# Optimization experiments

Hardware: AMD Instinct MI355X
Metric: run time of the kernel (lower is better)

The kernel has to match this reference:

```python
import jax, jax.numpy as jnp
import numpy as np

CUTOFF = 5.0
CUTOFF_ANGLE = 3.5
N = 25000
E = 800000
EA = 300000
T = 1600000
NBASIS = 8          # default radial basis size (bessel)
NBASIS_ANG = 8
DIM = 256
DIM_SRC = 64
DIM_DST = 32
DIM_ANGLE = 8
NMAX_ANGLE = 4
SPECIES_DIM = 16
NSPEC = 50


def bessel_basis(r, rc, n):
    # sin(k*pi*r/rc)/r Bessel-type radial basis, k=1..n  -> [E, n]
    x = r[:, None]
    k = jnp.arange(1, n + 1, dtype=r.dtype)[None, :] * (np.pi / rc)
    return jnp.sqrt(2.0 / rc) * jnp.sin(k * x) / x


def tssr2(x):
    # two-sided smooth square-root activation (identity inside |x|<=1)
    ax = jnp.abs(x)
    return jnp.where(ax <= 1.0, x, jnp.sign(x) * (2.0 * jnp.sqrt(jnp.maximum(ax, 1.0)) - 1.0))


def setup_inputs() -> dict:
    key = jax.random.key(0)
    ks = jax.random.split(key, 24)
    species = jax.random.randint(ks[0], (N,), 1, 17)
    edge_src = jax.random.randint(ks[1], (E,), 0, N)
    edge_dst = jax.random.randint(ks[2], (E,), 0, N)
    distances = 0.5 + jax.random.uniform(ks[3], (E,)) * (CUTOFF - 0.5)
    switch = 0.5 + 0.5 * jnp.cos(np.pi * distances / CUTOFF)
    angles = jax.random.uniform(ks[4], (T,)) * np.pi
    angle_src = jax.random.randint(ks[5], (T,), 0, EA)
    angle_dst = jax.random.randint(ks[6], (T,), 0, EA)
    central_atom = jax.random.randint(ks[7], (T,), 0, N)
    distances_angle = 0.5 + jax.random.uniform(ks[8], (EA,)) * (CUTOFF_ANGLE - 0.5)
    switch_angle = 0.5 + 0.5 * jnp.cos(np.pi * distances_angle / CUTOFF_ANGLE)
    s = lambda k, sh, scale: jax.random.normal(k, sh, jnp.float32) * scale
    din0 = SPECIES_DIM + DIM_SRC + NBASIS * DIM_DST + (NMAX_ANGLE + 1) * DIM_ANGLE  # 376
    din1 = DIM + DIM_SRC + NBASIS * DIM_DST + (NMAX_ANGLE + 1) * DIM_ANGLE          # 616
    return {
        'species': species, 'edge_src': edge_src, 'edge_dst': edge_dst,
        'distances': distances, 'switch': switch,
        'angles': angles, 'angle_src': angle_src, 'angle_dst': angle_dst,
        'central_atom': central_atom, 'distances_angle': distances_angle,
        'switch_angle': switch_angle,
        'species_table': s(ks[9], (NSPEC, SPECIES_DIM), 1.0),
        'W_si0': s(ks[10], (SPECIES_DIM, DIM_SRC + DIM_DST), SPECIES_DIM ** -0.5),
        'W_si1': s(ks[11], (DIM, DIM_SRC + DIM_DST), DIM ** -0.5),
        'W_da0': s(ks[12], (NBASIS_ANG, DIM_ANGLE), NBASIS_ANG ** -0.5),
        'W_da1': s(ks[13], (NBASIS_ANG, DIM_ANGLE), NBASIS_ANG ** -0.5),
        'W_mix0': s(ks[14], (din0, DIM), din0 ** -0.5),
        'b_mix0': jnp.zeros((DIM,), jnp.float32),
        'W_mix1': s(ks[15], (din1, DIM), din1 ** -0.5),
        'b_mix1': jnp.zeros((DIM,), jnp.float32),
    }


def reference(species, edge_src, edge_dst, distances, switch, angles, angle_src,
              angle_dst, central_atom, distances_angle, switch_angle,
              species_table, W_si0, W_si1, W_da0, W_da1,
              W_mix0, b_mix0, W_mix1, b_mix1):
    n_atoms = species.shape[0]
    # species encoding (learned/random table lookup)
    xi = species_table[species]                                   # [N, 16]
    # radial embeddings, smoothly switched at cutoff
    rb = bessel_basis(distances, CUTOFF, NBASIS) * switch[:, None]            # [E, 8]
    rba = bessel_basis(distances_angle, CUTOFF_ANGLE, NBASIS_ANG) * switch_angle[:, None]  # [EA, 8]
    # fourier angular features cos(n*theta), n=0..nmax_angle
    nvec = jnp.arange(NMAX_ANGLE + 1, dtype=angles.dtype)[None, :]
    xa = jnp.cos(nvec * angles[:, None])                          # [T, 5]
    for W_si, W_da, W_mix, b_mix in ((W_si0, W_da0, W_mix0, b_mix0),
                                     (W_si1, W_da1, W_mix1, b_mix1)):
        s = xi @ W_si                                             # [N, 96]
        si, si_dst = s[:, :DIM_SRC], s[:, DIM_SRC:]
        # radial message passing: outer(radial_basis, neighbor features) -> scatter-add
        mij = (rb[:, :, None] * si_dst[edge_dst][:, None, :]).reshape(rb.shape[0], -1)  # [E, 256]
        mi = jax.ops.segment_sum(mij, edge_src, num_segments=n_atoms)                   # [N, 256]
        # angular triplet features: pairwise vectors combined per angle
        da = rba @ W_da                                           # [EA, 8]
        dij = da[angle_src] * da[angle_dst]                       # [T, 8]
        ang = (xa[:, :, None] * dij[:, None, :]).reshape(xa.shape[0], -1)               # [T, 40]
        ami = jax.ops.segment_sum(ang, central_atom, num_segments=n_atoms)              # [N, 40]
        # mixing network + tssr2 mixing activation, residual when shapes match
        ei = jnp.concatenate([xi, si, mi, ami], axis=-1)
        dxi = tssr2(ei @ W_mix + b_mix)
        xi = xi + dxi if xi.shape[-1] == dxi.shape[-1] else dxi
    return xi
```

## Files before the change

### kernel.cpp

```cpp
#include <hip/hip_runtime.h>
#include <hip/hip_bf16.h>

typedef __hip_bfloat16 bf16;
typedef __bf16 bf8 __attribute__((ext_vector_type(8)));
typedef float  f4  __attribute__((ext_vector_type(4)));

#define N_ATOMS 25000
#define NE      800000
#define NEA     300000
#define NT      1600000
#define APB     64
#define NBUK    ((N_ATOMS + APB - 1) / APB)

#define DIN0  376
#define DIN1  616
#define DINP0 384
#define DINP1 640

#define EBLK ((NE + 4095) / 4096)
#define TBLK ((NT + 4095) / 4096)

#define NFRAG0 ((DINP0 / 32) * 16 * 64)
#define NFRAG1 ((DINP1 / 32) * 16 * 64)
#define NFRAGS (8 * 6 * 64)

#define S0BLK ((N_ATOMS * 120 + 255) / 256)
#define DABLK ((NEA + 255) / 256)

#define MIBLK ((N_ATOMS + 1) / 2)

__device__ __forceinline__ float tssr2f(float x) {
    float ax = fabsf(x);
    return (ax <= 1.f) ? x : copysignf(2.f * __builtin_sqrtf(ax) - 1.f, x);
}

__device__ __forceinline__ unsigned short f2bf_rn(float v) {
    unsigned int b = __float_as_uint(v);
    b += 0x7FFF + ((b >> 16) & 1);
    return (unsigned short)(b >> 16);
}
__device__ __forceinline__ float bf2f(unsigned short u) {
    return __uint_as_float(((unsigned int)u) << 16);
}

__global__ __launch_bounds__(256) void k_bcount(const int* __restrict__ esrc,
                                                const int* __restrict__ cat,
                                                int* __restrict__ ebcnt,
                                                int* __restrict__ tbcnt) {
    __shared__ int h[NBUK];
    int t = threadIdx.x;
    for (int b = t; b < NBUK; b += 256) h[b] = 0;
    __syncthreads();
    bool isE = blockIdx.x < EBLK;
    const int* key = isE ? esrc : cat;
    int n = isE ? NE : NT;
    int base = (isE ? blockIdx.x : (blockIdx.x - EBLK)) * 4096;
#pragma unroll
    for (int k = 0; k < 16; k++) {
        int idx = base + k * 256 + t;
        if (idx < n) atomicAdd(&h[key[idx] >> 6], 1);
    }
    __syncthreads();
    int* g = isE ? ebcnt : tbcnt;
    for (int b = t; b < NBUK; b += 256)
        if (h[b]) atomicAdd(&g[b], h[b]);
}

__global__ __launch_bounds__(512) void k_scanB(const int* cnt0, int* off0, int* cur0,
                                               int* aoff0,
                                               const int* cnt1, int* off1, int* cur1,
                                               int* aoff1) {
    const int* cnt = blockIdx.x ? cnt1 : cnt0;
    int* off  = blockIdx.x ? off1 : off0;
    int* cur  = blockIdx.x ? cur1 : cur0;
    int* aoff = blockIdx.x ? aoff1 : aoff0;
    int nelem = blockIdx.x ? NT : NE;
    __shared__ int sh[512];
    int t = threadIdx.x;
    int v = (t < NBUK) ? cnt[t] : 0;
    sh[t] = v;
    __syncthreads();
    for (int d = 1; d < 512; d <<= 1) {
        int a = (t >= d) ? sh[t - d] : 0;
        __syncthreads();
        sh[t] += a;
        __syncthreads();
    }
    int excl = sh[t] - v;
    if (t <= NBUK) { off[t] = excl; if (t < NBUK) cur[t] = excl; }
    if (t == 0) aoff[N_ATOMS] = nelem;
}

__global__ __launch_bounds__(512) void k_binA2(const float* __restrict__ eA,
                                               const float* __restrict__ eB,
                                               const int* __restrict__ eC,
                                               const int* __restrict__ ekey,
                                               int* __restrict__ egcur,
                                               float4* __restrict__ ebuk,
                                               const float* __restrict__ tA,
                                               const int* __restrict__ tB,
                                               const int* __restrict__ tC,
                                               const int* __restrict__ tkey,
                                               int* __restrict__ tgcur,
                                               float4* __restrict__ tbuk) {
    __shared__ int cnt[NBUK];
    __shared__ int rbase[NBUK];
    int t = threadIdx.x;
    for (int b = t; b < NBUK; b += 512) cnt[b] = 0;
    __syncthreads();
    bool isE = blockIdx.x < EBLK;
    const int* key = isE ? ekey : tkey;
    int n = isE ? NE : NT;
    int* gcur = isE ? egcur : tgcur;
    float4* buk = isE ? ebuk : tbuk;
    int base = (isE ? blockIdx.x : (blockIdx.x - EBLK)) * 4096;
    float4 pay[8];
    int bk[8], off[8];
#pragma unroll
    for (int k = 0; k < 8; k++) {
        int idx = base + k * 512 + t;
        bk[k] = -1;
        if (idx < n) {
            float4 p;
            if (isE) {
                p.x = eA[idx];
                p.y = eB[idx];
                p.z = __int_as_float(eC[idx]);
            } else {
                p.x = __cosf(tA[idx]);
                p.y = __int_as_float(tB[idx]);
                p.z = __int_as_float(tC[idx]);
            }
            int ky = key[idx];
            p.w = __int_as_float(ky);
            pay[k] = p;
            bk[k] = ky >> 6;
            off[k] = atomicAdd(&cnt[bk[k]], 1);
        }
    }
    __syncthreads();
    for (int b = t; b < NBUK; b += 512)
        if (cnt[b]) rbase[b] = atomicAdd(&gcur[b], cnt[b]);
    __syncthreads();
#pragma unroll
    for (int k = 0; k < 8; k++)
        if (bk[k] >= 0) buk[rbase[bk[k]] + off[k]] = pay[k];
}

__global__ __launch_bounds__(256) void k_binB2(const int* __restrict__ ebkoff,
                                               const float4* __restrict__ ebuk,
                                               float* __restrict__ erb,
                                               int* __restrict__ edi,
                                               int* __restrict__ eoff,
                                               const int* __restrict__ tbkoff,
                                               const float4* __restrict__ tbuk,
                                               float4* __restrict__ tfin,
                                               int* __restrict__ toff) {
    bool isE = blockIdx.x < NBUK;
    int b = isE ? blockIdx.x : (blockIdx.x - NBUK);
    const int* bkoff = isE ? ebkoff : tbkoff;
    const float4* buk = isE ? ebuk : tbuk;
    int* aoff = isE ? eoff : toff;
    int lo = b * APB;
    int hi = min(lo + APB, N_ATOMS);
    __shared__ int cnt[APB];
    __shared__ int cur[APB];
    int t = threadIdx.x;
    if (t < APB) cnt[t] = 0;
    __syncthreads();
    int pbeg = bkoff[b], pend = bkoff[b + 1];
    for (int p = pbeg + t; p < pend; p += 256) {
        int a = __float_as_int(((const float*)(buk + p))[3]);
        atomicAdd(&cnt[a - lo], 1);
    }
    __syncthreads();
    if (t == 0) {
        int run = pbeg;
        for (int k = 0; k < hi - lo; k++) {
            cur[k] = run;
            aoff[lo + k] = run;
            run += cnt[k];
        }
    }
    __syncthreads();
    for (int p = pbeg + t; p < pend; p += 256) {
        float4 pay = buk[p];
        int a = __float_as_int(pay.w);
        int slot = atomicAdd(&cur[a - lo], 1);
        if (isE) {
            float d = pay.x, s = pay.y;
            float q = 0.6324555320f * s / d;
            float r[8];
#pragma unroll
            for (int n = 0; n < 8; n++)
                r[n] = q * __sinf((n + 1) * 0.6283185307f * d);
            *(float4*)&erb[(size_t)slot * 8]     = make_float4(r[0], r[1], r[2], r[3]);
            *(float4*)&erb[(size_t)slot * 8 + 4] = make_float4(r[4], r[5], r[6], r[7]);
            edi[slot] = __float_as_int(pay.z);
        } else {
            tfin[slot] = pay;
        }
    }
}

__device__ __forceinline__ void wprep_one(const float* __restrict__ W, bf8* __restrict__ Wf,
                                          int K, int N, int ntiles, int f) {
    int lane = f & 63;
    int ft = f >> 6;
    int tile = ft % ntiles;
    int chunk = ft / ntiles;
    int n = tile * 16 + (lane & 15);
    int kb = chunk * 32 + (lane >> 4) * 8;
    bf8 v;
#pragma unroll
    for (int j = 0; j < 8; j++) {
        int k = kb + j;
        v[j] = (__bf16)((k < K) ? W[k * N + n] : 0.f);
    }
    Wf[f] = v;
}

__global__ __launch_bounds__(256) void k_wprep3(const float* __restrict__ W0, bf8* __restrict__ Wf0,
                                                const float* __restrict__ W1, bf8* __restrict__ Wf1,
                                                const float* __restrict__ WS, bf8* __restrict__ WfS) {
    int f = blockIdx.x * 256 + threadIdx.x;
    if (f < NFRAG0) {
        wprep_one(W0, Wf0, DIN0, 256, 16, f);
    } else if (f < NFRAG0 + NFRAG1) {
        wprep_one(W1, Wf1, DIN1, 256, 16, f - NFRAG0);
    } else if (f < NFRAG0 + NFRAG1 + NFRAGS) {
        wprep_one(WS, WfS, 256, 96, 6, f - NFRAG0 - NFRAG1);
    }
}

__global__ __launch_bounds__(256) void k_pre(const int* __restrict__ sp,
                                             const float* __restrict__ table,
                                             const float* __restrict__ W,
                                             unsigned short* __restrict__ ei0,
                                             float* __restrict__ sd,
                                             const float* __restrict__ dist,
                                             const float* __restrict__ sw,
                                             const float* __restrict__ Wda0,
                                             const float* __restrict__ Wda1,
                                             unsigned short* __restrict__ dah0,
                                             unsigned short* __restrict__ dah1) {
    if ((int)blockIdx.x < S0BLK) {
        int idx = blockIdx.x * 256 + threadIdx.x;
        if (idx >= N_ATOMS * 120) return;
        int i = idx / 120;
        int c = idx - i * 120;
        if (c >= 112) {
            ei0[(size_t)i * DINP0 + 376 + (c - 112)] = 0;
            return;
        }
        int s = sp[i];
        if (c < 16) {
            ei0[(size_t)i * DINP0 + c] = f2bf_rn(table[s * 16 + c]);
        } else {
            int cc = c - 16;
            float acc = 0.f;
#pragma unroll
            for (int k = 0; k < 16; k++)
                acc += table[s * 16 + k] * W[k * 96 + cc];
            if (cc < 64) ei0[(size_t)i * DINP0 + 16 + cc] = f2bf_rn(acc);
            else         sd[i * 32 + cc - 64]             = acc;
        }
    } else {
        int e = (blockIdx.x - S0BLK) * 256 + threadIdx.x;
        if (e >= NEA) return;
        float d = dist[e];
        float s = sw[e];
        float rb[8];
#pragma unroll
        for (int n = 0; n < 8; n++)
            rb[n] = 0.7559289460f * __sinf((n + 1) * 0.8975979010f * d) / d * s;
        unsigned short h0[8], h1[8];
#pragma unroll
        for (int c = 0; c < 8; c++) {
            float a0 = 0.f, a1 = 0.f;
#pragma unroll
            for (int n = 0; n < 8; n++) {
                a0 += rb[n] * Wda0[n * 8 + c];
                a1 += rb[n] * Wda1[n * 8 + c];
            }
            h0[c] = f2bf_rn(a0);
            h1[c] = f2bf_rn(a1);
        }
        *(uint4*)&dah0[e * 8] = *(uint4*)h0;
        *(uint4*)&dah1[e * 8] = *(uint4*)h1;
    }
}

__global__ __launch_bounds__(256) void k_s1(const unsigned short* __restrict__ ei1,
                                            const bf8* __restrict__ Wf,
                                            unsigned short* __restrict__ ei1o,
                                            float* __restrict__ sd) {
    __shared__ __align__(16) __bf16 Asg[4][64][8];
    int t = threadIdx.x;
    int w = t >> 6, lane = t & 63;
    int a0 = blockIdx.x * 64;

    int satom = a0 + (t >> 2);
    int k8 = (t & 3) * 8;
    const unsigned short* arow = &ei1[(size_t)satom * DINP1 + k8];
    bool aok = satom < N_ATOMS;
    int dw = (t >> 2) >> 4;
    int dl = ((t >> 2) & 15) | ((t & 3) << 4);
    __bf16* adst = &Asg[dw][dl][0];

    f4 acc[6];
#pragma unroll
    for (int j = 0; j < 6; j++) {
        f4 z = {0.f, 0.f, 0.f, 0.f};
        acc[j] = z;
    }

    for (int ch = 0; ch < 8; ch++) {
        uint4 v = make_uint4(0, 0, 0, 0);
        if (aok) v = *(const uint4*)(arow + ch * 32);
        __syncthreads();
        *(uint4*)adst = v;
        __syncthreads();
        bf8 afr = *(const bf8*)&Asg[w][lane][0];
        const bf8* wp = &Wf[(ch * 6) * 64 + lane];
#pragma unroll
        for (int tn = 0; tn < 6; tn++) {
            bf8 b = wp[tn * 64];
            acc[tn] = __builtin_amdgcn_mfma_f32_16x16x32_bf16(afr, b, acc[tn], 0, 0, 0);
        }
    }

    int nlo = lane & 15, q = lane >> 4;
#pragma unroll
    for (int r = 0; r < 4; r++) {
        int atom = a0 + w * 16 + q * 4 + r;
        if (atom < N_ATOMS) {
#pragma unroll
            for (int tn = 0; tn < 6; tn++) {
                int col = tn * 16 + nlo;
                float v = acc[tn][r];
                if (col < 64) ei1o[(size_t)atom * DINP1 + 256 + col] = f2bf_rn(v);
                else          sd[atom * 32 + col - 64] = v;
            }
        }
    }
    for (int z = t; z < 64 * 24; z += 256) {
        int za = a0 + z / 24;
        if (za < N_ATOMS) ei1o[(size_t)za * DINP1 + 616 + z % 24] = 0;
    }
}

__device__ __forceinline__ void ami_win(const float4 twA, const unsigned short* __restrict__ dah,
                                        int lim, int jj, int c,
                                        float& a0, float& a1, float& a2, float& a3, float& a4) {
    int gmax = (lim + 7) >> 3;
    float sc = 0.f; unsigned short dA = 0, dB = 0;
    {
        sc = __shfl(twA.x, jj, 64);
        int ea = __float_as_int(__shfl(twA.y, jj, 64));
        int eb = __float_as_int(__shfl(twA.z, jj, 64));
        dA = dah[ea * 8 + c];
        dB = dah[eb * 8 + c];
    }
    for (int g = 0; g < gmax; g++) {
        float scN = 0.f; unsigned short dAN = 0, dBN = 0;
        if (g + 1 < gmax) {
            int sl = (g + 1) * 8 + jj;
            scN = __shfl(twA.x, sl, 64);
            int ea = __float_as_int(__shfl(twA.y, sl, 64));
            int eb = __float_as_int(__shfl(twA.z, sl, 64));
            dAN = dah[ea * 8 + c];
            dBN = dah[eb * 8 + c];
        }
        float dij = bf2f(dA) * bf2f(dB);
        dij = (g * 8 + jj < lim) ? dij : 0.f;
        float c1 = sc;
        float c2 = __builtin_fmaf(2.f * c1, c1, -1.f);
        float c3 = __builtin_fmaf(2.f * c1, c2, -c1);
        float c4 = __builtin_fmaf(2.f * c1, c3, -c2);
        a0 += dij;
        a1 = __builtin_fmaf(c1, dij, a1);
        a2 = __builtin_fmaf(c2, dij, a2);
        a3 = __builtin_fmaf(c3, dij, a3);
        a4 = __builtin_fmaf(c4, dij, a4);
        if (g + 1 < gmax) { sc = scN; dA = dAN; dB = dBN; }
    }
}

__global__ __launch_bounds__(256) void k_seg(const int* __restrict__ eoff,
                                             const float* __restrict__ erb,
                                             const int* __restrict__ edi,
                                             const float* __restrict__ sd,
                                             unsigned short* __restrict__ mo, int mstride,
                                             const int* __restrict__ toff,
                                             const float4* __restrict__ tpay,
                                             const unsigned short* __restrict__ dah,
                                             unsigned short* __restrict__ ao, int astride) {
    __shared__ float4 smi[2][64];
    __shared__ float  sam[2][5][8];
    int t = threadIdx.x;
    int wv = t >> 6, l = t & 63;
    int slot = wv >> 1;
    int p    = wv & 1;

    if ((int)blockIdx.x < MIBLK) {
        int i = blockIdx.x * 2 + slot;
        bool valid = (i < N_ATOMS);
        int beg = 0, end = 0;
        if (valid) { beg = toff[i]; end = toff[i + 1]; }
        int cnt = end - beg;
        int jj = l >> 3, c = l & 7;
        float a0 = 0.f, a1 = 0.f, a2 = 0.f, a3 = 0.f, a4 = 0.f;

        if (cnt > 0) {
            if (cnt <= 128) {
                int nG = (cnt + 7) >> 3;
                int h0 = (nG + 1) >> 1;
                int tb = p ? h0 * 8 : 0;
                int te = p ? cnt : min(h0 * 8, cnt);
                int mycnt = te - tb;
                if (mycnt > 0) {
                    float4 twA = tpay[beg + tb + min(l, mycnt - 1)];
                    ami_win(twA, dah, mycnt, jj, c, a0, a1, a2, a3, a4);
                }
            } else {
                int nW = (cnt + 63) >> 6;
                for (int W = p; W < nW; W += 2) {
                    int wbase = W * 64;
                    int rem = cnt - wbase;
                    int lim = min(rem, 64);
                    float4 twA = tpay[beg + wbase + min(l, rem - 1)];
                    ami_win(twA, dah, lim, jj, c, a0, a1, a2, a3, a4);
                }
            }
        }

#pragma unroll
        for (int msk = 8; msk <= 32; msk <<= 1) {
            a0 += __shfl_xor(a0, msk, 64);
            a1 += __shfl_xor(a1, msk, 64);
            a2 += __shfl_xor(a2, msk, 64);
            a3 += __shfl_xor(a3, msk, 64);
            a4 += __shfl_xor(a4, msk, 64);
        }
        if (p == 1 && l < 8) {
            sam[slot][0][l] = a0; sam[slot][1][l] = a1; sam[slot][2][l] = a2;
            sam[slot][3][l] = a3; sam[slot][4][l] = a4;
        }
        __syncthreads();
        if (valid && p == 0 && l < 8) {
            a0 += sam[slot][0][l]; a1 += sam[slot][1][l]; a2 += sam[slot][2][l];
            a3 += sam[slot][3][l]; a4 += sam[slot][4][l];
            unsigned short* o = &ao[(size_t)i * astride + c];
            o[0]  = f2bf_rn(a0);
            o[8]  = f2bf_rn(a1);
            o[16] = f2bf_rn(a2);
            o[24] = f2bf_rn(a3);
            o[32] = f2bf_rn(a4);
        }
    } else {
        int i = ((int)blockIdx.x - MIBLK) * 2 + slot;
        bool valid = (i < N_ATOMS);
        int beg = 0, end = 0;
        if (valid) { beg = eoff[i]; end = eoff[i + 1]; }
        int cnt = end - beg;
        int n = l >> 3, cb = (l & 7) * 4;
        float4 acc = make_float4(0.f, 0.f, 0.f, 0.f);

        if (cnt > 0) {
            int nG = (cnt + 7) >> 3;
            int h0 = (nG + 1) >> 1;
            int gbeg = p ? h0 : 0;
            int gend = p ? nG : h0;
            if (cnt <= 64) {
                int eWin = edi[beg + min(l, cnt - 1)];
                int cmax = end * 8 - 1;
                if (gbeg < gend) {
                    float cA = erb[min((beg + gbeg * 8) * 8 + l, cmax)];
                    for (int g = gbeg; g < gend; g++) {
                        int e8 = g * 8;
                        float4 v[8];
#pragma unroll
                        for (int j = 0; j < 8; j++) {
                            int eid = __shfl(eWin, e8 + j, 64);
                            v[j] = *(const float4*)&sd[eid * 32 + cb];
                        }
                        float cB = 0.f;
                        if (g + 1 < gend) cB = erb[min((beg + e8 + 8) * 8 + l, cmax)];
#pragma unroll
                        for (int j = 0; j < 8; j++) {
                            float r_ = __shfl(cA, j * 8 + n, 64);
                            r_ = (e8 + j < cnt) ? r_ : 0.f;
                            acc.x += r_ * v[j].x; acc.y += r_ * v[j].y;
                            acc.z += r_ * v[j].z; acc.w += r_ * v[j].w;
                        }
                        if (g + 1 < gend) cA = cB;
                    }
                }
            } else {
                const float* rp = erb + (size_t)beg * 8 + n;
                const int*   dp = edi + beg;
                for (int g = gbeg; g < gend; g++) {
                    int e8 = g * 8;
                    int m = cnt - e8;
#pragma unroll
                    for (int j = 0; j < 8; j++) {
                        int jj = min(j, m - 1);
                        float rb = rp[(e8 + jj) * 8];
                        int di = dp[e8 + jj];
                        if (j >= m) rb = 0.f;
                        float4 v = *(const float4*)&sd[di * 32 + cb];
                        acc.x += rb * v.x; acc.y += rb * v.y;
                        acc.z += rb * v.z; acc.w += rb * v.w;
                    }
                }
            }
        }

        if (p == 1) smi[slot][l] = acc;
        __syncthreads();
        if (valid && p == 0) {
            float4 o = smi[slot][l];
            acc.x += o.x; acc.y += o.y; acc.z += o.z; acc.w += o.w;
            ushort4 pk = make_ushort4(f2bf_rn(acc.x), f2bf_rn(acc.y),
                                      f2bf_rn(acc.z), f2bf_rn(acc.w));
            *(ushort4*)&mo[(size_t)i * mstride + l * 4] = pk;
        }
    }
}

template <int LAYER>
__global__ __launch_bounds__(256) void k_gemm(const unsigned short* __restrict__ ei,
                                              const bf8* __restrict__ Wf,
                                              const float* __restrict__ bias,
                                              const unsigned short* __restrict__ skip,
                                              float* __restrict__ outf,
                                              unsigned short* __restrict__ outb) {
    constexpr int DINP = (LAYER == 0) ? DINP0 : DINP1;
    constexpr int NCH = DINP / 32;
    __shared__ __align__(16) __bf16 Asg[2][64][8];
    int t = threadIdx.x;
    int w = t >> 6, lane = t & 63;
    int a0 = blockIdx.x * 32;

    int f  = t * 4;
    int tA = f >> 9;
    int al = (f >> 3) & 63;
    int j0 = f & 7;
    int sm = al & 15, sq = al >> 4;
    int ga = a0 + tA * 16 + sm;
    const unsigned short* arow = &ei[(size_t)ga * DINP + sq * 8 + j0];
    __bf16* adst = &Asg[0][0][0] + f;
    bool aok = (ga < N_ATOMS);

    f4 acc[2][4];
#pragma unroll
    for (int i = 0; i < 2; i++)
#pragma unroll
        for (int j = 0; j < 4; j++) {
            f4 z = {0.f, 0.f, 0.f, 0.f};
            acc[i][j] = z;
        }

    for (int ch = 0; ch < NCH; ch++) {
        uint2 v = make_uint2(0, 0);
        if (aok) v = *(const uint2*)(arow + ch * 32);
        __syncthreads();
        *(uint2*)adst = v;
        __syncthreads();
        bf8 afr0 = *(const bf8*)&Asg[0][lane][0];
        bf8 afr1 = *(const bf8*)&Asg[1][lane][0];
        const bf8* wp = &Wf[(ch * 16 + w * 4) * 64 + lane];
#pragma unroll
        for (int tn = 0; tn < 4; tn++) {
            bf8 b = wp[tn * 64];
            acc[0][tn] = __builtin_amdgcn_mfma_f32_16x16x32_bf16(afr0, b, acc[0][tn], 0, 0, 0);
            acc[1][tn] = __builtin_amdgcn_mfma_f32_16x16x32_bf16(afr1, b, acc[1][tn], 0, 0, 0);
        }
    }

    int nlo = lane & 15, q = lane >> 4;
#pragma unroll
    for (int tA2 = 0; tA2 < 2; tA2++) {
#pragma unroll
        for (int r = 0; r < 4; r++) {
            int atom = a0 + tA2 * 16 + q * 4 + r;
            if (atom < N_ATOMS) {
#pragma unroll
                for (int tn = 0; tn < 4; tn++) {
                    int col = w * 64 + tn * 16 + nlo;
                    float vv = tssr2f(acc[tA2][tn][r] + bias[col]);
                    if (LAYER == 0) {
                        outb[(size_t)atom * DINP1 + col] = f2bf_rn(vv);
                    } else {
                        outf[(size_t)atom * 256 + col] =
                            vv + bf2f(skip[(size_t)atom * DINP1 + col]);
                    }
                }
            }
        }
    }
}

extern "C" void kernel_launch(void* const* d_in, const int* in_sizes, int n_in,
                              void* d_out, int out_size, void* d_ws, size_t ws_size,
                              hipStream_t stream) {
    const int*   species     = (const int*)d_in[0];
    const int*   edge_src    = (const int*)d_in[1];
    const int*   edge_dst    = (const int*)d_in[2];
    const float* distances   = (const float*)d_in[3];
    const float* sw          = (const float*)d_in[4];
    const float* angles      = (const float*)d_in[5];
    const int*   angle_src   = (const int*)d_in[6];
    const int*   angle_dst   = (const int*)d_in[7];
    const int*   central     = (const int*)d_in[8];
    const float* dist_a      = (const float*)d_in[9];
    const float* sw_a        = (const float*)d_in[10];
    const float* table       = (const float*)d_in[11];
    const float* W_si0       = (const float*)d_in[12];
    const float* W_si1       = (const float*)d_in[13];
    const float* W_da0       = (const float*)d_in[14];
    const float* W_da1       = (const float*)d_in[15];
    const float* W_mix0      = (const float*)d_in[16];
    const float* b_mix0      = (const float*)d_in[17];
    const float* W_mix1      = (const float*)d_in[18];
    const float* b_mix1      = (const float*)d_in[19];
    float* out = (float*)d_out;

    char* p = (char*)d_ws;
    auto alloc = [&](size_t bytes) {
        char* r = p;
        p += (bytes + 255) & ~(size_t)255;
        return (void*)r;
    };
    unsigned short* ei0 = (unsigned short*)alloc((size_t)N_ATOMS * DINP0 * 2);
    unsigned short* ei1 = (unsigned short*)alloc((size_t)N_ATOMS * DINP1 * 2);
    float*  sd   = (float*)alloc((size_t)N_ATOMS * 32 * 4);
    unsigned short* dah0 = (unsigned short*)alloc((size_t)NEA * 8 * 2);
    unsigned short* dah1 = (unsigned short*)alloc((size_t)NEA * 8 * 2);
    float*  erbf = (float*)alloc((size_t)NE * 8 * 4);
    int*    edi  = (int*)alloc((size_t)NE * 4);
    float4* tpay = (float4*)alloc((size_t)NT * 16);
    bf8*    Wf0  = (bf8*)alloc((size_t)NFRAG0 * 16);
    bf8*    Wf1  = (bf8*)alloc((size_t)NFRAG1 * 16);
    bf8*    WfS1 = (bf8*)alloc((size_t)NFRAGS * 16);
    int* eoff   = (int*)alloc((size_t)(N_ATOMS + 1) * 4);
    int* toff   = (int*)alloc((size_t)(N_ATOMS + 1) * 4);
    int* bcnt   = (int*)alloc((size_t)2 * NBUK * 4);
    int* ebkoff = (int*)alloc((size_t)(NBUK + 1) * 4);
    int* tbkoff = (int*)alloc((size_t)(NBUK + 1) * 4);
    int* gce    = (int*)alloc((size_t)NBUK * 4);
    int* gct    = (int*)alloc((size_t)NBUK * 4);
    (void)ws_size;
    int* ebcnt = bcnt;
    int* tbcnt = bcnt + NBUK;

    float4* ebuk = (float4*)ei0;
    float4* tbuk = (float4*)ei1;

    hipMemsetAsync(bcnt, 0, (size_t)2 * NBUK * 4, stream);

    k_wprep3<<<(NFRAG0 + NFRAG1 + NFRAGS + 255) / 256, 256, 0, stream>>>(
        W_mix0, Wf0, W_mix1, Wf1, W_si1, WfS1);

    k_bcount<<<EBLK + TBLK, 256, 0, stream>>>(edge_src, central, ebcnt, tbcnt);
    k_scanB<<<2, 512, 0, stream>>>(ebcnt, ebkoff, gce, eoff, tbcnt, tbkoff, gct, toff);

    k_binA2<<<EBLK + TBLK, 512, 0, stream>>>(
        distances, sw, edge_dst, edge_src, gce, ebuk,
        angles, angle_src, angle_dst, central, gct, tbuk);
    k_binB2<<<2 * NBUK, 256, 0, stream>>>(
        ebkoff, ebuk, erbf, edi, eoff,
        tbkoff, tbuk, tpay, toff);

    k_pre<<<S0BLK + DABLK, 256, 0, stream>>>(
        species, table, W_si0, ei0, sd,
        dist_a, sw_a, W_da0, W_da1, dah0, dah1);

    int gemm_grid = (N_ATOMS + 31) / 32;

    k_seg<<<2 * MIBLK, 256, 0, stream>>>(eoff, erbf, edi, sd, ei0 + 80, DINP0,
                                         toff, tpay, dah0, ei0 + 336, DINP0);
    k_gemm<0><<<gemm_grid, 256, 0, stream>>>(ei0, Wf0, b_mix0, nullptr, nullptr, ei1);

    k_s1<<<(N_ATOMS + 63) / 64, 256, 0, stream>>>(ei1, WfS1, ei1, sd);
    k_seg<<<2 * MIBLK, 256, 0, stream>>>(eoff, erbf, edi, sd, ei1 + 320, DINP1,
                                         toff, tpay, dah1, ei1 + 576, DINP1);
    k_gemm<1><<<gemm_grid, 256, 0, stream>>>(ei1, Wf1, b_mix1, ei1, out, nullptr);
}
```

Baseline: 412.2 us.

## Pad per-atom segments to multiples of 8 and fuse preprocessing kernels

Counts elements per atom rather than per bucket, then scans padded (multiple-of-8) per-atom offsets. The second binning pass can then place each atom's edges into padded segments filled with zero/dummy entries. The segment-sum kernels drop their tail masking and clamping and use vectorized radial-basis loads over full groups of 8. Weight prep is merged with counting, and binning with the species/angle preprocessing, to cut launches. The cost is extra padded storage and traffic, a separate bucket buffer, and per-atom global atomics during counting.

```diff
diff --git a/kernel.cpp b/kernel.cpp
--- a/kernel.cpp
+++ b/kernel.cpp
@@ -23,9 +23,12 @@
 #define NFRAG0 ((DINP0 / 32) * 16 * 64)
 #define NFRAG1 ((DINP1 / 32) * 16 * 64)
 #define NFRAGS (8 * 6 * 64)
-
-#define S0BLK ((N_ATOMS * 120 + 255) / 256)
-#define DABLK ((NEA + 255) / 256)
+#define WBLK   ((NFRAG0 + NFRAG1 + NFRAGS + 255) / 256)
+
+#define S0BLK2 ((N_ATOMS * 120 + 511) / 512)
+#define DABLK2 ((NEA + 1 + 511) / 512)
+
+#define SCH ((N_ATOMS + 511) / 512)
 
 #define MIBLK ((N_ATOMS + 1) / 2)
 
@@ -41,166 +44,6 @@
 }
 __device__ __forceinline__ float bf2f(unsigned short u) {
     return __uint_as_float(((unsigned int)u) << 16);
-}
-
-__global__ __launch_bounds__(256) void k_bcount(const int* __restrict__ esrc,
-                                                const int* __restrict__ cat,
-                                                int* __restrict__ ebcnt,
-                                                int* __restrict__ tbcnt) {
-    __shared__ int h[NBUK];
-    int t = threadIdx.x;
-    for (int b = t; b < NBUK; b += 256) h[b] = 0;
-    __syncthreads();
-    bool isE = blockIdx.x < EBLK;
-    const int* key = isE ? esrc : cat;
-    int n = isE ? NE : NT;
-    int base = (isE ? blockIdx.x : (blockIdx.x - EBLK)) * 4096;
-#pragma unroll
-    for (int k = 0; k < 16; k++) {
-        int idx = base + k * 256 + t;
-        if (idx < n) atomicAdd(&h[key[idx] >> 6], 1);
-    }
-    __syncthreads();
-    int* g = isE ? ebcnt : tbcnt;
-    for (int b = t; b < NBUK; b += 256)
-        if (h[b]) atomicAdd(&g[b], h[b]);
-}
-
-__global__ __launch_bounds__(512) void k_scanB(const int* cnt0, int* off0, int* cur0,
-                                               int* aoff0,
-                                               const int* cnt1, int* off1, int* cur1,
-                                               int* aoff1) {
-    const int* cnt = blockIdx.x ? cnt1 : cnt0;
-    int* off  = blockIdx.x ? off1 : off0;
-    int* cur  = blockIdx.x ? cur1 : cur0;
-    int* aoff = blockIdx.x ? aoff1 : aoff0;
-    int nelem = blockIdx.x ? NT : NE;
-    __shared__ int sh[512];
-    int t = threadIdx.x;
-    int v = (t < NBUK) ? cnt[t] : 0;
-    sh[t] = v;
-    __syncthreads();
-    for (int d = 1; d < 512; d <<= 1) {
-        int a = (t >= d) ? sh[t - d] : 0;
-        __syncthreads();
-        sh[t] += a;
-        __syncthreads();
-    }
-    int excl = sh[t] - v;
-    if (t <= NBUK) { off[t] = excl; if (t < NBUK) cur[t] = excl; }
-    if (t == 0) aoff[N_ATOMS] = nelem;
-}
-
-__global__ __launch_bounds__(512) void k_binA2(const float* __restrict__ eA,
-                                               const float* __restrict__ eB,
-                                               const int* __restrict__ eC,
-                                               const int* __restrict__ ekey,
-                                               int* __restrict__ egcur,
-                                               float4* __restrict__ ebuk,
-                                               const float* __restrict__ tA,
-                                               const int* __restrict__ tB,
-                                               const int* __restrict__ tC,
-                                               const int* __restrict__ tkey,
-                                               int* __restrict__ tgcur,
-                                               float4* __restrict__ tbuk) {
-    __shared__ int cnt[NBUK];
-    __shared__ int rbase[NBUK];
-    int t = threadIdx.x;
-    for (int b = t; b < NBUK; b += 512) cnt[b] = 0;
-    __syncthreads();
-    bool isE = blockIdx.x < EBLK;
-    const int* key = isE ? ekey : tkey;
-    int n = isE ? NE : NT;
-    int* gcur = isE ? egcur : tgcur;
-    float4* buk = isE ? ebuk : tbuk;
-    int base = (isE ? blockIdx.x : (blockIdx.x - EBLK)) * 4096;
-    float4 pay[8];
-    int bk[8], off[8];
-#pragma unroll
-    for (int k = 0; k < 8; k++) {
-        int idx = base + k * 512 + t;
-        bk[k] = -1;
-        if (idx < n) {
-            float4 p;
-            if (isE) {
-                p.x = eA[idx];
-                p.y = eB[idx];
-                p.z = __int_as_float(eC[idx]);
-            } else {
-                p.x = __cosf(tA[idx]);
-                p.y = __int_as_float(tB[idx]);
-                p.z = __int_as_float(tC[idx]);
-            }
-            int ky = key[idx];
-            p.w = __int_as_float(ky);
-            pay[k] = p;
-            bk[k] = ky >> 6;
-            off[k] = atomicAdd(&cnt[bk[k]], 1);
-        }
-    }
-    __syncthreads();
-    for (int b = t; b < NBUK; b += 512)
-        if (cnt[b]) rbase[b] = atomicAdd(&gcur[b], cnt[b]);
-    __syncthreads();
-#pragma unroll
-    for (int k = 0; k < 8; k++)
-        if (bk[k] >= 0) buk[rbase[bk[k]] + off[k]] = pay[k];
-}
-
-__global__ __launch_bounds__(256) void k_binB2(const int* __restrict__ ebkoff,
-                                               const float4* __restrict__ ebuk,
-                                               float* __restrict__ erb,
-                                               int* __restrict__ edi,
-                                               int* __restrict__ eoff,
-                                               const int* __restrict__ tbkoff,
-                                               const float4* __restrict__ tbuk,
-                                               float4* __restrict__ tfin,
-                                               int* __restrict__ toff) {
-    bool isE = blockIdx.x < NBUK;
-    int b = isE ? blockIdx.x : (blockIdx.x - NBUK);
-    const int* bkoff = isE ? ebkoff : tbkoff;
-    const float4* buk = isE ? ebuk : tbuk;
-    int* aoff = isE ? eoff : toff;
-    int lo = b * APB;
-    int hi = min(lo + APB, N_ATOMS);
-    __shared__ int cnt[APB];
-    __shared__ int cur[APB];
-    int t = threadIdx.x;
-    if (t < APB) cnt[t] = 0;
-    __syncthreads();
-    int pbeg = bkoff[b], pend = bkoff[b + 1];
-    for (int p = pbeg + t; p < pend; p += 256) {
-        int a = __float_as_int(((const float*)(buk + p))[3]);
-        atomicAdd(&cnt[a - lo], 1);
-    }
-    __syncthreads();
-    if (t == 0) {
-        int run = pbeg;
-        for (int k = 0; k < hi - lo; k++) {
-            cur[k] = run;
-            aoff[lo + k] = run;
-            run += cnt[k];
-        }
-    }
-    __syncthreads();
-    for (int p = pbeg + t; p < pend; p += 256) {
-        float4 pay = buk[p];
-        int a = __float_as_int(pay.w);
-        int slot = atomicAdd(&cur[a - lo], 1);
-        if (isE) {
-            float d = pay.x, s = pay.y;
-            float q = 0.6324555320f * s / d;
-            float r[8];
-#pragma unroll
-            for (int n = 0; n < 8; n++)
-                r[n] = q * __sinf((n + 1) * 0.6283185307f * d);
-            *(float4*)&erb[(size_t)slot * 8]     = make_float4(r[0], r[1], r[2], r[3]);
-            *(float4*)&erb[(size_t)slot * 8 + 4] = make_float4(r[4], r[5], r[6], r[7]);
-            edi[slot] = __float_as_int(pay.z);
-        } else {
-            tfin[slot] = pay;
-        }
-    }
 }
 
 __device__ __forceinline__ void wprep_one(const float* __restrict__ W, bf8* __restrict__ Wf,
@@ -220,32 +63,133 @@
     Wf[f] = v;
 }
 
-__global__ __launch_bounds__(256) void k_wprep3(const float* __restrict__ W0, bf8* __restrict__ Wf0,
-                                                const float* __restrict__ W1, bf8* __restrict__ Wf1,
-                                                const float* __restrict__ WS, bf8* __restrict__ WfS) {
-    int f = blockIdx.x * 256 + threadIdx.x;
-    if (f < NFRAG0) {
-        wprep_one(W0, Wf0, DIN0, 256, 16, f);
-    } else if (f < NFRAG0 + NFRAG1) {
-        wprep_one(W1, Wf1, DIN1, 256, 16, f - NFRAG0);
-    } else if (f < NFRAG0 + NFRAG1 + NFRAGS) {
-        wprep_one(WS, WfS, 256, 96, 6, f - NFRAG0 - NFRAG1);
-    }
-}
-
-__global__ __launch_bounds__(256) void k_pre(const int* __restrict__ sp,
-                                             const float* __restrict__ table,
-                                             const float* __restrict__ W,
-                                             unsigned short* __restrict__ ei0,
-                                             float* __restrict__ sd,
-                                             const float* __restrict__ dist,
-                                             const float* __restrict__ sw,
-                                             const float* __restrict__ Wda0,
-                                             const float* __restrict__ Wda1,
-                                             unsigned short* __restrict__ dah0,
-                                             unsigned short* __restrict__ dah1) {
-    if ((int)blockIdx.x < S0BLK) {
-        int idx = blockIdx.x * 256 + threadIdx.x;
+__global__ __launch_bounds__(256) void k_wc(const float* __restrict__ W0, bf8* __restrict__ Wf0,
+                                            const float* __restrict__ W1, bf8* __restrict__ Wf1,
+                                            const float* __restrict__ WS, bf8* __restrict__ WfS,
+                                            const int* __restrict__ esrc, const int* __restrict__ cat,
+                                            int* __restrict__ acnt, int* __restrict__ tcnt) {
+    int bid = blockIdx.x;
+    if (bid < WBLK) {
+        int f = bid * 256 + threadIdx.x;
+        if (f < NFRAG0) {
+            wprep_one(W0, Wf0, DIN0, 256, 16, f);
+        } else if (f < NFRAG0 + NFRAG1) {
+            wprep_one(W1, Wf1, DIN1, 256, 16, f - NFRAG0);
+        } else if (f < NFRAG0 + NFRAG1 + NFRAGS) {
+            wprep_one(WS, WfS, 256, 96, 6, f - NFRAG0 - NFRAG1);
+        }
+        return;
+    }
+    bid -= WBLK;
+    bool isE = bid < EBLK;
+    const int* key = isE ? esrc : cat;
+    int n = isE ? NE : NT;
+    int* cp = isE ? acnt : tcnt;
+    int base = (isE ? bid : bid - EBLK) * 4096;
+    int t = threadIdx.x;
+#pragma unroll
+    for (int k = 0; k < 16; k++) {
+        int idx = base + k * 256 + t;
+        if (idx < n) atomicAdd(&cp[key[idx]], 1);
+    }
+}
+
+__global__ __launch_bounds__(512) void k_scanA(const int* __restrict__ acnt, int* __restrict__ epoff,
+                                               int* __restrict__ gce,
+                                               const int* __restrict__ tcnt, int* __restrict__ tpoff,
+                                               int* __restrict__ gct) {
+    const int* cnt = blockIdx.x ? tcnt : acnt;
+    int* off = blockIdx.x ? tpoff : epoff;
+    int* gc  = blockIdx.x ? gct : gce;
+    __shared__ int sh[512];
+    int t = threadIdx.x;
+    int i0 = t * SCH, i1 = min(i0 + SCH, N_ATOMS);
+    int s = 0;
+    for (int i = i0; i < i1; i++) s += (cnt[i] + 7) & ~7;
+    sh[t] = s;
+    __syncthreads();
+    for (int d = 1; d < 512; d <<= 1) {
+        int a = (t >= d) ? sh[t - d] : 0;
+        __syncthreads();
+        sh[t] += a;
+        __syncthreads();
+    }
+    int run = sh[t] - s;
+    for (int i = i0; i < i1; i++) { off[i] = run; run += (cnt[i] + 7) & ~7; }
+    if (t == 0) off[N_ATOMS] = sh[511];
+    __syncthreads();
+    for (int b = t; b < NBUK; b += 512) gc[b] = off[b * APB];
+}
+
+__global__ __launch_bounds__(512) void k_bpre(const float* __restrict__ eA,
+                                              const float* __restrict__ eB,
+                                              const int* __restrict__ eC,
+                                              const int* __restrict__ ekey,
+                                              int* __restrict__ egcur,
+                                              float4* __restrict__ ebuk,
+                                              const float* __restrict__ tA,
+                                              const int* __restrict__ tB,
+                                              const int* __restrict__ tC,
+                                              const int* __restrict__ tkey,
+                                              int* __restrict__ tgcur,
+                                              float4* __restrict__ tbuk,
+                                              const int* __restrict__ sp,
+                                              const float* __restrict__ table,
+                                              const float* __restrict__ Wsi,
+                                              unsigned short* __restrict__ ei0,
+                                              float* __restrict__ sd,
+                                              const float* __restrict__ dist,
+                                              const float* __restrict__ sw2,
+                                              const float* __restrict__ Wda0,
+                                              const float* __restrict__ Wda1,
+                                              unsigned short* __restrict__ dah0,
+                                              unsigned short* __restrict__ dah1) {
+    int bid = blockIdx.x;
+    int t = threadIdx.x;
+    if (bid < EBLK + TBLK) {
+        __shared__ int cnt[NBUK];
+        __shared__ int rbase[NBUK];
+        for (int b = t; b < NBUK; b += 512) cnt[b] = 0;
+        __syncthreads();
+        bool isE = bid < EBLK;
+        const int* key = isE ? ekey : tkey;
+        int n = isE ? NE : NT;
+        int* gcur = isE ? egcur : tgcur;
+        float4* buk = isE ? ebuk : tbuk;
+        int base = (isE ? bid : (bid - EBLK)) * 4096;
+        float4 pay[8];
+        int bk[8], off[8];
+#pragma unroll
+        for (int k = 0; k < 8; k++) {
+            int idx = base + k * 512 + t;
+            bk[k] = -1;
+            if (idx < n) {
+                float4 p;
+                if (isE) {
+                    p.x = eA[idx];
+                    p.y = eB[idx];
+                    p.z = __int_as_float(eC[idx]);
+                } else {
+                    p.x = __cosf(tA[idx]);
+                    p.y = __int_as_float(tB[idx]);
+                    p.z = __int_as_float(tC[idx]);
+                }
+                int ky = key[idx];
+                p.w = __int_as_float(ky);
+                pay[k] = p;
+                bk[k] = ky >> 6;
+                off[k] = atomicAdd(&cnt[bk[k]], 1);
+            }
+        }
+        __syncthreads();
+        for (int b = t; b < NBUK; b += 512)
+            if (cnt[b]) rbase[b] = atomicAdd(&gcur[b], cnt[b]);
+        __syncthreads();
+#pragma unroll
+        for (int k = 0; k < 8; k++)
+            if (bk[k] >= 0) buk[rbase[bk[k]] + off[k]] = pay[k];
+    } else if (bid < EBLK + TBLK + S0BLK2) {
+        int idx = (bid - EBLK - TBLK) * 512 + t;
         if (idx >= N_ATOMS * 120) return;
         int i = idx / 120;
         int c = idx - i * 120;
@@ -261,15 +205,21 @@
             float acc = 0.f;
 #pragma unroll
             for (int k = 0; k < 16; k++)
-                acc += table[s * 16 + k] * W[k * 96 + cc];
+                acc += table[s * 16 + k] * Wsi[k * 96 + cc];
             if (cc < 64) ei0[(size_t)i * DINP0 + 16 + cc] = f2bf_rn(acc);
             else         sd[i * 32 + cc - 64]             = acc;
         }
     } else {
-        int e = (blockIdx.x - S0BLK) * 256 + threadIdx.x;
-        if (e >= NEA) return;
+        int e = (bid - EBLK - TBLK - S0BLK2) * 512 + t;
+        if (e > NEA) return;
+        if (e == NEA) {
+            uint4 z = make_uint4(0, 0, 0, 0);
+            *(uint4*)&dah0[(size_t)e * 8] = z;
+            *(uint4*)&dah1[(size_t)e * 8] = z;
+            return;
+        }
         float d = dist[e];
-        float s = sw[e];
+        float s = sw2[e];
         float rb[8];
 #pragma unroll
         for (int n = 0; n < 8; n++)
@@ -288,6 +238,70 @@
         }
         *(uint4*)&dah0[e * 8] = *(uint4*)h0;
         *(uint4*)&dah1[e * 8] = *(uint4*)h1;
+    }
+}
+
+__global__ __launch_bounds__(256) void k_binB2(const int* __restrict__ epoff,
+                                               const int* __restrict__ acnt,
+                                               const int* __restrict__ gce,
+                                               const float4* __restrict__ ebuk,
+                                               float* __restrict__ erb,
+                                               int* __restrict__ edi,
+                                               const int* __restrict__ tpoff,
+                                               const int* __restrict__ tcnt,
+                                               const int* __restrict__ gct,
+                                               const float4* __restrict__ tbuk,
+                                               float4* __restrict__ tpay) {
+    bool isE = blockIdx.x < NBUK;
+    int b = isE ? blockIdx.x : (blockIdx.x - NBUK);
+    const int* off  = isE ? epoff : tpoff;
+    const int* cntA = isE ? acnt : tcnt;
+    const int* gfin = isE ? gce : gct;
+    const float4* buk = isE ? ebuk : tbuk;
+    int lo = b * APB;
+    int hi = min(lo + APB, N_ATOMS);
+    __shared__ int abase[APB];
+    __shared__ int cur[APB];
+    int t = threadIdx.x;
+    if (t < hi - lo) {
+        int base = off[lo + t];
+        int pe   = off[lo + t + 1];
+        int c    = cntA[lo + t];
+        abase[t] = base;
+        cur[t]   = base;
+        if (isE) {
+            for (int s = base + c; s < pe; s++) {
+                edi[s] = 0;
+                int pos = s - base;
+                float* dz = erb + ((size_t)base + (pos & ~7)) * 8 + (pos & 7);
+#pragma unroll
+                for (int nn = 0; nn < 8; nn++) dz[nn * 8] = 0.f;
+            }
+        } else {
+            float4 pz = make_float4(0.f, __int_as_float(NEA), __int_as_float(NEA), 0.f);
+            for (int s = base + c; s < pe; s++) tpay[s] = pz;
+        }
+    }
+    __syncthreads();
+    int pstart = off[lo];
+    int pend = gfin[b];
+    for (int p = pstart + t; p < pend; p += 256) {
+        float4 pay = buk[p];
+        int a = __float_as_int(pay.w);
+        int k = a - lo;
+        int slot = atomicAdd(&cur[k], 1);
+        if (isE) {
+            float d = pay.x, s2 = pay.y;
+            float q = 0.6324555320f * s2 / d;
+            int pos = slot - abase[k];
+            float* dst = erb + ((size_t)abase[k] + (pos & ~7)) * 8 + (pos & 7);
+#pragma unroll
+            for (int nn = 0; nn < 8; nn++)
+                dst[nn * 8] = q * __sinf((nn + 1) * 0.6283185307f * d);
+            edi[slot] = __float_as_int(pay.z);
+        } else {
+            tpay[slot] = pay;
+        }
     }
 }
 
@@ -351,9 +365,8 @@
 }
 
 __device__ __forceinline__ void ami_win(const float4 twA, const unsigned short* __restrict__ dah,
-                                        int lim, int jj, int c,
+                                        int gmax, int jj, int c,
                                         float& a0, float& a1, float& a2, float& a3, float& a4) {
-    int gmax = (lim + 7) >> 3;
     float sc = 0.f; unsigned short dA = 0, dB = 0;
     {
         sc = __shfl(twA.x, jj, 64);
@@ -373,7 +386,6 @@
             dBN = dah[eb * 8 + c];
         }
         float dij = bf2f(dA) * bf2f(dB);
-        dij = (g * 8 + jj < lim) ? dij : 0.f;
         float c1 = sc;
         float c2 = __builtin_fmaf(2.f * c1, c1, -1.f);
         float c3 = __builtin_fmaf(2.f * c1, c2, -c1);
@@ -406,31 +418,31 @@
     if ((int)blockIdx.x < MIBLK) {
         int i = blockIdx.x * 2 + slot;
         bool valid = (i < N_ATOMS);
-        int beg = 0, end = 0;
-        if (valid) { beg = toff[i]; end = toff[i + 1]; }
-        int cnt = end - beg;
+        int pbeg = 0, pend = 0;
+        if (valid) { pbeg = toff[i]; pend = toff[i + 1]; }
+        int pcnt = pend - pbeg;
         int jj = l >> 3, c = l & 7;
         float a0 = 0.f, a1 = 0.f, a2 = 0.f, a3 = 0.f, a4 = 0.f;
 
-        if (cnt > 0) {
-            if (cnt <= 128) {
-                int nG = (cnt + 7) >> 3;
+        if (pcnt > 0) {
+            int nG = pcnt >> 3;
+            if (pcnt <= 128) {
                 int h0 = (nG + 1) >> 1;
-                int tb = p ? h0 * 8 : 0;
-                int te = p ? cnt : min(h0 * 8, cnt);
-                int mycnt = te - tb;
-                if (mycnt > 0) {
-                    float4 twA = tpay[beg + tb + min(l, mycnt - 1)];
-                    ami_win(twA, dah, mycnt, jj, c, a0, a1, a2, a3, a4);
+                int gb = p ? h0 : 0;
+                int myg = p ? (nG - h0) : h0;
+                if (myg > 0) {
+                    int tb = gb * 8;
+                    float4 twA = tpay[pbeg + tb + min(l, myg * 8 - 1)];
+                    ami_win(twA, dah, myg, jj, c, a0, a1, a2, a3, a4);
                 }
             } else {
-                int nW = (cnt + 63) >> 6;
+                int nW = (pcnt + 63) >> 6;
                 for (int W = p; W < nW; W += 2) {
                     int wbase = W * 64;
-                    int rem = cnt - wbase;
+                    int rem = pcnt - wbase;
                     int lim = min(rem, 64);
-                    float4 twA = tpay[beg + wbase + min(l, rem - 1)];
-                    ami_win(twA, dah, lim, jj, c, a0, a1, a2, a3, a4);
+                    float4 twA = tpay[pbeg + wbase + min(l, rem - 1)];
+                    ami_win(twA, dah, lim >> 3, jj, c, a0, a1, a2, a3, a4);
                 }
             }
         }
@@ -461,57 +473,53 @@
     } else {
         int i = ((int)blockIdx.x - MIBLK) * 2 + slot;
         bool valid = (i < N_ATOMS);
-        int beg = 0, end = 0;
-        if (valid) { beg = eoff[i]; end = eoff[i + 1]; }
-        int cnt = end - beg;
+        int pbeg = 0, pend = 0;
+        if (valid) { pbeg = eoff[i]; pend = eoff[i + 1]; }
+        int pcnt = pend - pbeg;
         int n = l >> 3, cb = (l & 7) * 4;
         float4 acc = make_float4(0.f, 0.f, 0.f, 0.f);
 
-        if (cnt > 0) {
-            int nG = (cnt + 7) >> 3;
+        if (pcnt > 0) {
+            int nG = pcnt >> 3;
             int h0 = (nG + 1) >> 1;
             int gbeg = p ? h0 : 0;
             int gend = p ? nG : h0;
-            if (cnt <= 64) {
-                int eWin = edi[beg + min(l, cnt - 1)];
-                int cmax = end * 8 - 1;
-                if (gbeg < gend) {
-                    float cA = erb[min((beg + gbeg * 8) * 8 + l, cmax)];
-                    for (int g = gbeg; g < gend; g++) {
-                        int e8 = g * 8;
-                        float4 v[8];
-#pragma unroll
-                        for (int j = 0; j < 8; j++) {
-                            int eid = __shfl(eWin, e8 + j, 64);
-                            v[j] = *(const float4*)&sd[eid * 32 + cb];
-                        }
-                        float cB = 0.f;
-                        if (g + 1 < gend) cB = erb[min((beg + e8 + 8) * 8 + l, cmax)];
-#pragma unroll
-                        for (int j = 0; j < 8; j++) {
-                            float r_ = __shfl(cA, j * 8 + n, 64);
-                            r_ = (e8 + j < cnt) ? r_ : 0.f;
-                            acc.x += r_ * v[j].x; acc.y += r_ * v[j].y;
-                            acc.z += r_ * v[j].z; acc.w += r_ * v[j].w;
-                        }
-                        if (g + 1 < gend) cA = cB;
+            if (pcnt <= 64) {
+                int eWin = edi[pbeg + min(l, pcnt - 1)];
+                for (int g = gbeg; g < gend; g++) {
+                    const float* rp = erb + ((size_t)pbeg + g * 8) * 8 + n * 8;
+                    f4 rA = *(const f4*)rp;
+                    f4 rB = *(const f4*)(rp + 4);
+                    float4 v[8];
+#pragma unroll
+                    for (int j = 0; j < 8; j++) {
+                        int eid = __shfl(eWin, g * 8 + j, 64);
+                        v[j] = *(const float4*)&sd[eid * 32 + cb];
+                    }
+#pragma unroll
+                    for (int j = 0; j < 8; j++) {
+                        float rbj = (j < 4) ? rA[j] : rB[j - 4];
+                        acc.x += rbj * v[j].x; acc.y += rbj * v[j].y;
+                        acc.z += rbj * v[j].z; acc.w += rbj * v[j].w;
                     }
                 }
             } else {
-                const float* rp = erb + (size_t)beg * 8 + n;
-                const int*   dp = edi + beg;
+                const int* dp = edi + pbeg;
                 for (int g = gbeg; g < gend; g++) {
-                    int e8 = g * 8;
-                    int m = cnt - e8;
+                    const float* rp = erb + ((size_t)pbeg + g * 8) * 8 + n * 8;
+                    f4 rA = *(const f4*)rp;
+                    f4 rB = *(const f4*)(rp + 4);
+                    float4 v[8];
 #pragma unroll
                     for (int j = 0; j < 8; j++) {
-                        int jj = min(j, m - 1);
-                        float rb = rp[(e8 + jj) * 8];
-                        int di = dp[e8 + jj];
-                        if (j >= m) rb = 0.f;
-                        float4 v = *(const float4*)&sd[di * 32 + cb];
-                        acc.x += rb * v.x; acc.y += rb * v.y;
-                        acc.z += rb * v.z; acc.w += rb * v.w;
+                        int eid = dp[g * 8 + j];
+                        v[j] = *(const float4*)&sd[eid * 32 + cb];
+                    }
+#pragma unroll
+                    for (int j = 0; j < 8; j++) {
+                        float rbj = (j < 4) ? rA[j] : rB[j - 4];
+                        acc.x += rbj * v[j].x; acc.y += rbj * v[j].y;
+                        acc.z += rbj * v[j].z; acc.w += rbj * v[j].w;
                     }
                 }
             }
@@ -636,55 +644,52 @@
     unsigned short* ei0 = (unsigned short*)alloc((size_t)N_ATOMS * DINP0 * 2);
     unsigned short* ei1 = (unsigned short*)alloc((size_t)N_ATOMS * DINP1 * 2);
     float*  sd   = (float*)alloc((size_t)N_ATOMS * 32 * 4);
-    unsigned short* dah0 = (unsigned short*)alloc((size_t)NEA * 8 * 2);
-    unsigned short* dah1 = (unsigned short*)alloc((size_t)NEA * 8 * 2);
-    float*  erbf = (float*)alloc((size_t)NE * 8 * 4);
-    int*    edi  = (int*)alloc((size_t)NE * 4);
-    float4* tpay = (float4*)alloc((size_t)NT * 16);
+    unsigned short* dah0 = (unsigned short*)alloc((size_t)(NEA + 1) * 8 * 2);
+    unsigned short* dah1 = (unsigned short*)alloc((size_t)(NEA + 1) * 8 * 2);
+    float*  erbf = (float*)alloc((size_t)(NE + 8 * N_ATOMS) * 8 * 4);
+    int*    edi  = (int*)alloc((size_t)(NE + 8 * N_ATOMS) * 4);
+    float4* tpay = (float4*)alloc((size_t)(NT + 8 * N_ATOMS) * 16);
+    float4* ebuk = (float4*)alloc((size_t)(NE + 8 * N_ATOMS) * 16);
     bf8*    Wf0  = (bf8*)alloc((size_t)NFRAG0 * 16);
     bf8*    Wf1  = (bf8*)alloc((size_t)NFRAG1 * 16);
     bf8*    WfS1 = (bf8*)alloc((size_t)NFRAGS * 16);
-    int* eoff   = (int*)alloc((size_t)(N_ATOMS + 1) * 4);
-    int* toff   = (int*)alloc((size_t)(N_ATOMS + 1) * 4);
-    int* bcnt   = (int*)alloc((size_t)2 * NBUK * 4);
-    int* ebkoff = (int*)alloc((size_t)(NBUK + 1) * 4);
-    int* tbkoff = (int*)alloc((size_t)(NBUK + 1) * 4);
+    int* epoff  = (int*)alloc((size_t)(N_ATOMS + 1) * 4);
+    int* tpoff  = (int*)alloc((size_t)(N_ATOMS + 1) * 4);
+    int* cnts   = (int*)alloc((size_t)2 * N_ATOMS * 4);
     int* gce    = (int*)alloc((size_t)NBUK * 4);
     int* gct    = (int*)alloc((size_t)NBUK * 4);
     (void)ws_size;
-    int* ebcnt = bcnt;
-    int* tbcnt = bcnt + NBUK;
-
-    float4* ebuk = (float4*)ei0;
+    int* acnt = cnts;
+    int* tcnt = cnts + N_ATOMS;
+
     float4* tbuk = (float4*)ei1;
 
-    hipMemsetAsync(bcnt, 0, (size_t)2 * NBUK * 4, stream);
-
-    k_wprep3<<<(NFRAG0 + NFRAG1 + NFRAGS + 255) / 256, 256, 0, stream>>>(
-        W_mix0, Wf0, W_mix1, Wf1, W_si1, WfS1);
-
-    k_bcount<<<EBLK + TBLK, 256, 0, stream>>>(edge_src, central, ebcnt, tbcnt);
-    k_scanB<<<2, 512, 0, stream>>>(ebcnt, ebkoff, gce, eoff, tbcnt, tbkoff, gct, toff);
-
-    k_binA2<<<EBLK + TBLK, 512, 0, stream>>>(
+    hipMemsetAsync(cnts, 0, (size_t)2 * N_ATOMS * 4, stream);
+
+    k_wc<<<WBLK + EBLK + TBLK, 256, 0, stream>>>(
+        W_mix0, Wf0, W_mix1, Wf1, W_si1, WfS1,
+        edge_src, central, acnt, tcnt);
+
+    k_scanA<<<2, 512, 0, stream>>>(acnt, epoff, gce, tcnt, tpoff, gct);
+
+    k_bpre<<<EBLK + TBLK + S0BLK2 + DABLK2, 512, 0, stream>>>(
         distances, sw, edge_dst, edge_src, gce, ebuk,
-        angles, angle_src, angle_dst, central, gct, tbuk);
-    k_binB2<<<2 * NBUK, 256, 0, stream>>>(
-        ebkoff, ebuk, erbf, edi, eoff,
-        tbkoff, tbuk, tpay, toff);
-
-    k_pre<<<S0BLK + DABLK, 256, 0, stream>>>(
+        angles, angle_src, angle_dst, central, gct, tbuk,
         species, table, W_si0, ei0, sd,
         dist_a, sw_a, W_da0, W_da1, dah0, dah1);
 
+    k_binB2<<<2 * NBUK, 256, 0, stream>>>(
+        epoff, acnt, gce, ebuk, erbf, edi,
+        tpoff, tcnt, gct, tbuk, tpay);
+
     int gemm_grid = (N_ATOMS + 31) / 32;
 
-    k_seg<<<2 * MIBLK, 256, 0, stream>>>(eoff, erbf, edi, sd, ei0 + 80, DINP0,
-                                         toff, tpay, dah0, ei0 + 336, DINP0);
+    k_seg<<<2 * MIBLK, 256, 0, stream>>>(epoff, erbf, edi, sd, ei0 + 80, DINP0,
+                                         tpoff, tpay, dah0, ei0 + 336, DINP0);
     k_gemm<0><<<gemm_grid, 256, 0, stream>>>(ei0, Wf0, b_mix0, nullptr, nullptr, ei1);
 
     k_s1<<<(N_ATOMS + 63) / 64, 256, 0, stream>>>(ei1, WfS1, ei1, sd);
-    k_seg<<<2 * MIBLK, 256, 0, stream>>>(eoff, erbf, edi, sd, ei1 + 320, DINP1,
-                                         toff, tpay, dah1, ei1 + 576, DINP1);
+    k_seg<<<2 * MIBLK, 256, 0, stream>>>(epoff, erbf, edi, sd, ei1 + 320, DINP1,
+                                         tpoff, tpay, dah1, ei1 + 576, DINP1);
     k_gemm<1><<<gemm_grid, 256, 0, stream>>>(ei1, Wf1, b_mix1, ei1, out, nullptr);
 }
```

New measurement: 538.9 us. +30.7%, slower.
